# Kernel tuning notes

Hardware: AMD Instinct MI355X
Metric: run time of the kernel (lower is better)

The kernel has to match this reference:

```python
import jax, jax.numpy as jnp
import numpy as np

NUM_FORMULAS = 1024
INPUT_DIM = 256
BATCH = 2048


def setup_inputs() -> dict:
    key = jax.random.key(0)
    k_x, k_mu, k_sigma = jax.random.split(key, 3)
    inputs = jax.random.normal(k_x, (BATCH, INPUT_DIM), dtype=jnp.float32)
    # keras random_normal initializer default stddev = 0.05
    mu = 0.05 * jax.random.normal(k_mu, (NUM_FORMULAS, INPUT_DIM), dtype=jnp.float32)
    sigma = 0.05 * jax.random.normal(k_sigma, (1, NUM_FORMULAS, INPUT_DIM), dtype=jnp.float32)
    temperature = jnp.float32(2.0)
    return {"inputs": inputs, "mu": mu, "sigma": sigma, "temperature": temperature}


def reference(inputs, mu, sigma, temperature):
    # diff: (batch, num_formulas, dim)
    diff = inputs[:, None, :] - mu[None, :, :]
    # weighted L2 norm over feature dim -> (batch, num_formulas)
    dist = jnp.sqrt(jnp.sum(jnp.square(diff * sigma), axis=-1))
    loc = jnp.exp(-dist)
    # sigmoid-gated temperature, softmax over formulas (last axis)
    return jax.nn.softmax(jax.nn.sigmoid(temperature) * loc, axis=-1)
```

## Files before the change

kernel.cpp:

```cpp
#include <hip/hip_runtime.h>
#include <math.h>

#define NF 1024
#define DIM 256
#define BATCH 2048
#define K 512
#define BM 64
#define BN 64
#define KB 64
#define NCHUNK (NF / BN)

#define WS_A_BYTES (BATCH * K * 2)
#define WS_B_OFF   WS_A_BYTES
#define WS_C_OFF   (WS_A_BYTES + NF * K * 2)
#define WS_RP_OFF  (WS_C_OFF + NF * 4)

typedef __attribute__((ext_vector_type(8))) short short8;
typedef __attribute__((ext_vector_type(4))) float f32x4;

__device__ __forceinline__ unsigned short f2bf(float f) {
    unsigned u = __float_as_uint(f);
    u += 0x7fffu + ((u >> 16) & 1u);
    return (unsigned short)(u >> 16);
}

__device__ __forceinline__ void gl_lds16(const ushort* g, ushort* l) {
    __builtin_amdgcn_global_load_lds(
        (const __attribute__((address_space(1))) void*)g,
        (__attribute__((address_space(3))) void*)l, 16, 0, 0);
}

__global__ __launch_bounds__(256) void k_prep(const float* __restrict__ mu,
                                              const float* __restrict__ sigma,
                                              const float* __restrict__ x,
                                              unsigned int* __restrict__ Ab32,
                                              unsigned int* __restrict__ Bb32,
                                              float* __restrict__ c) {
    const int t = threadIdx.x;
    if (blockIdx.x >= NF) {
        const int i = (blockIdx.x - NF) * 256 + t;
        const float v = x[i];
        Ab32[i] = (unsigned)f2bf(v * v) | ((unsigned)f2bf(v) << 16);
        return;
    }
    const int f = blockIdx.x;
    const float m = mu[f * DIM + t];
    const float s = sigma[f * DIM + t];
    const float s2 = s * s;
    Bb32[f * DIM + t] = (unsigned)f2bf(s2) | ((unsigned)f2bf(-2.0f * s2 * m) << 16);

    float cp = s2 * m * m;
    #pragma unroll
    for (int off = 32; off > 0; off >>= 1) cp += __shfl_down(cp, off, 64);
    __shared__ float red[4];
    const int lane = t & 63, wv = t >> 6;
    if (lane == 0) red[wv] = cp;
    __syncthreads();
    if (t == 0) c[f] = red[0] + red[1] + red[2] + red[3];
}

__global__ __launch_bounds__(256, 2) void k_main(const ushort* __restrict__ Ab,
                                                 const ushort* __restrict__ Bb,
                                                 const float* __restrict__ c,
                                                 const float* __restrict__ temp,
                                                 float* __restrict__ out,
                                                 float* __restrict__ rowPartial) {
    const int t = threadIdx.x;
    const int w = t >> 6;
    const int lane = t & 63;
    const int m16 = lane & 15;
    const int q = lane >> 4;
    const int wr = w >> 1, wc = w & 1;
    const int r0 = blockIdx.x * BM;
    const int n0 = blockIdx.y * BN;

    __shared__ __align__(16) ushort lds[8192];
    __shared__ float sums[4][32];

    f32x4 acc[2][2];
    #pragma unroll
    for (int rt = 0; rt < 2; ++rt)
        #pragma unroll
        for (int ct = 0; ct < 2; ++ct) acc[rt][ct] = (f32x4){0.f, 0.f, 0.f, 0.f};

    int srow[2], skc[2];
    #pragma unroll
    for (int h = 0; h < 2; ++h) {
        const int s = h * 256 + t;
        srow[h] = s >> 3;
        skc[h] = (s & 7) ^ (srow[h] & 7);
    }

    for (int kb = 0; kb < K; kb += KB) {
        __syncthreads();
        #pragma unroll
        for (int h = 0; h < 2; ++h) {
            const int s = h * 256 + t;
            gl_lds16(Ab + (r0 + srow[h]) * K + kb + skc[h] * 8, &lds[s * 8]);
            gl_lds16(Bb + (n0 + srow[h]) * K + kb + skc[h] * 8, &lds[4096 + s * 8]);
        }
        __syncthreads();

        #pragma unroll
        for (int ks = 0; ks < KB; ks += 32) {
            const int kcq = (ks >> 3) + q;
            short8 av[2], bv[2];
            #pragma unroll
            for (int j = 0; j < 2; ++j) {
                const int ar = wr * 32 + j * 16 + m16;
                av[j] = *(const short8*)&lds[(ar * 8 + (kcq ^ (ar & 7))) * 8];
                const int fr = wc * 32 + j * 16 + m16;
                bv[j] = *(const short8*)&lds[4096 + (fr * 8 + (kcq ^ (fr & 7))) * 8];
            }
            #pragma unroll
            for (int rt = 0; rt < 2; ++rt)
                #pragma unroll
                for (int ct = 0; ct < 2; ++ct)
                    acc[rt][ct] = __builtin_amdgcn_mfma_f32_16x16x32_bf16(
                        av[rt], bv[ct], acc[rt][ct], 0, 0, 0);
        }
    }

    const float g = 1.0f / (1.0f + __expf(-temp[0]));
    #pragma unroll
    for (int rt = 0; rt < 2; ++rt) {
        float s[4] = {0.f, 0.f, 0.f, 0.f};
        #pragma unroll
        for (int ct = 0; ct < 2; ++ct) {
            const int fcol = n0 + wc * 32 + ct * 16 + m16;
            const float cn = c[fcol];
            #pragma unroll
            for (int i = 0; i < 4; ++i) {
                const float dist2 = acc[rt][ct][i] + cn;
                const float dist = sqrtf(fmaxf(dist2, 0.0f));
                const float p = __expf(g * __expf(-dist));
                const int row = r0 + wr * 32 + rt * 16 + q * 4 + i;
                out[row * NF + fcol] = p;
                s[i] += p;
            }
        }
        #pragma unroll
        for (int i = 0; i < 4; ++i) {
            #pragma unroll
            for (int mask = 1; mask < 16; mask <<= 1)
                s[i] += __shfl_xor(s[i], mask, 64);
        }
        if (m16 == 0) {
            #pragma unroll
            for (int i = 0; i < 4; ++i) sums[w][rt * 16 + q * 4 + i] = s[i];
        }
    }
    __syncthreads();
    if (t < BM) {
        const int half = t >> 5, lr = t & 31;
        rowPartial[blockIdx.y * BATCH + r0 + t] =
            sums[half * 2][lr] + sums[half * 2 + 1][lr];
    }
}

__global__ __launch_bounds__(256) void k_norm(float* __restrict__ out,
                                              const float* __restrict__ rowPartial) {
    const int row = blockIdx.x;
    float ssum = 0.0f;
    #pragma unroll
    for (int ch = 0; ch < NCHUNK; ++ch) ssum += rowPartial[ch * BATCH + row];
    const float inv = 1.0f / ssum;
    float4* o4 = (float4*)(out + row * NF);
    float4 v = o4[threadIdx.x];
    v.x *= inv; v.y *= inv; v.z *= inv; v.w *= inv;
    o4[threadIdx.x] = v;
}

extern "C" void kernel_launch(void* const* d_in, const int* in_sizes, int n_in,
                              void* d_out, int out_size, void* d_ws, size_t ws_size,
                              hipStream_t stream) {
    const float* x     = (const float*)d_in[0];
    const float* mu    = (const float*)d_in[1];
    const float* sigma = (const float*)d_in[2];
    const float* temp  = (const float*)d_in[3];
    float* out = (float*)d_out;

    char* ws = (char*)d_ws;
    ushort* Ab        = (ushort*)ws;
    ushort* Bb        = (ushort*)(ws + WS_B_OFF);
    float*  c         = (float*)(ws + WS_C_OFF);
    float*  rowPartial = (float*)(ws + WS_RP_OFF);

    k_prep<<<NF + BATCH * DIM / 256, 256, 0, stream>>>(mu, sigma, x,
                                                       (unsigned int*)Ab,
                                                       (unsigned int*)Bb, c);

    dim3 g2(BATCH / BM, NF / BN);
    k_main<<<g2, 256, 0, stream>>>(Ab, Bb, c, temp, out, rowPartial);

    k_norm<<<BATCH, 256, 0, stream>>>(out, rowPartial);
}
```

Baseline: 80.26 us.

## Fuse softmax normalization into GEMM kernel with full-row blocks and in-kernel A conversion

Each block now computes 16 full output rows across all 1024 formulas, using 8 waves of 128 columns each. This lets the softmax row sum and normalization happen inside the kernel, which removes the separate normalize kernel and the extra read and rewrite of the output. The x-to-bf16 packing moves from the prep kernel into the main kernel's LDS staging. B operands are read straight from global memory into registers with double buffering instead of going through LDS tiles. The risk is heavy redundant B traffic (every block reads the whole 1 MB B), served by L2. There are also fewer blocks (128) than CUs, which may underfill the GPU.

```diff
diff --git a/kernel.cpp b/kernel.cpp
--- a/kernel.cpp
+++ b/kernel.cpp
@@ -5,15 +5,10 @@
 #define DIM 256
 #define BATCH 2048
 #define K 512
-#define BM 64
-#define BN 64
-#define KB 64
-#define NCHUNK (NF / BN)
+#define BMF 16
+#define GX (BATCH / BMF)
 
-#define WS_A_BYTES (BATCH * K * 2)
-#define WS_B_OFF   WS_A_BYTES
-#define WS_C_OFF   (WS_A_BYTES + NF * K * 2)
-#define WS_RP_OFF  (WS_C_OFF + NF * 4)
+#define WS_C_OFF (NF * K * 2)
 
 typedef __attribute__((ext_vector_type(8))) short short8;
 typedef __attribute__((ext_vector_type(4))) float f32x4;
@@ -24,25 +19,11 @@
     return (unsigned short)(u >> 16);
 }
 
-__device__ __forceinline__ void gl_lds16(const ushort* g, ushort* l) {
-    __builtin_amdgcn_global_load_lds(
-        (const __attribute__((address_space(1))) void*)g,
-        (__attribute__((address_space(3))) void*)l, 16, 0, 0);
-}
-
 __global__ __launch_bounds__(256) void k_prep(const float* __restrict__ mu,
                                               const float* __restrict__ sigma,
-                                              const float* __restrict__ x,
-                                              unsigned int* __restrict__ Ab32,
                                               unsigned int* __restrict__ Bb32,
                                               float* __restrict__ c) {
     const int t = threadIdx.x;
-    if (blockIdx.x >= NF) {
-        const int i = (blockIdx.x - NF) * 256 + t;
-        const float v = x[i];
-        Ab32[i] = (unsigned)f2bf(v * v) | ((unsigned)f2bf(v) << 16);
-        return;
-    }
     const int f = blockIdx.x;
     const float m = mu[f * DIM + t];
     const float s = sigma[f * DIM + t];
@@ -59,116 +40,131 @@
     if (t == 0) c[f] = red[0] + red[1] + red[2] + red[3];
 }
 
-__global__ __launch_bounds__(256, 2) void k_main(const ushort* __restrict__ Ab,
+__global__ __launch_bounds__(512, 2) void k_full(const float* __restrict__ x,
                                                  const ushort* __restrict__ Bb,
                                                  const float* __restrict__ c,
                                                  const float* __restrict__ temp,
-                                                 float* __restrict__ out,
-                                                 float* __restrict__ rowPartial) {
+                                                 float* __restrict__ out) {
     const int t = threadIdx.x;
     const int w = t >> 6;
     const int lane = t & 63;
     const int m16 = lane & 15;
     const int q = lane >> 4;
-    const int wr = w >> 1, wc = w & 1;
-    const int r0 = blockIdx.x * BM;
-    const int n0 = blockIdx.y * BN;
+    const int r0 = blockIdx.x * BMF;
 
-    __shared__ __align__(16) ushort lds[8192];
-    __shared__ float sums[4][32];
+    __shared__ __align__(16) ushort ldsA[BMF * K];
+    __shared__ float wsum[8][BMF];
+    __shared__ float rowInv[BMF];
 
-    f32x4 acc[2][2];
-    #pragma unroll
-    for (int rt = 0; rt < 2; ++rt)
-        #pragma unroll
-        for (int ct = 0; ct < 2; ++ct) acc[rt][ct] = (f32x4){0.f, 0.f, 0.f, 0.f};
-
-    int srow[2], skc[2];
     #pragma unroll
     for (int h = 0; h < 2; ++h) {
-        const int s = h * 256 + t;
-        srow[h] = s >> 3;
-        skc[h] = (s & 7) ^ (srow[h] & 7);
+        const int u = h * 512 + t;
+        const int row = u >> 6, kc = u & 63;
+        const float4 v = *(const float4*)&x[(r0 + row) * DIM + kc * 4];
+        uint4 pk;
+        pk.x = (unsigned)f2bf(v.x * v.x) | ((unsigned)f2bf(v.x) << 16);
+        pk.y = (unsigned)f2bf(v.y * v.y) | ((unsigned)f2bf(v.y) << 16);
+        pk.z = (unsigned)f2bf(v.z * v.z) | ((unsigned)f2bf(v.z) << 16);
+        pk.w = (unsigned)f2bf(v.w * v.w) | ((unsigned)f2bf(v.w) << 16);
+        *(uint4*)&ldsA[(row * 64 + (kc ^ (row & 7))) * 8] = pk;
     }
+    __syncthreads();
 
-    for (int kb = 0; kb < K; kb += KB) {
-        __syncthreads();
+    f32x4 acc[8];
+    #pragma unroll
+    for (int ct = 0; ct < 8; ++ct) acc[ct] = (f32x4){0.f, 0.f, 0.f, 0.f};
+
+    const ushort* bbase = Bb + (w * 128 + m16) * K + q * 8;
+
+    short8 b0[8], b1[8];
+    #pragma unroll
+    for (int ct = 0; ct < 8; ++ct)
+        b0[ct] = *(const short8*)(bbase + ct * 16 * K);
+
+    #pragma unroll 1
+    for (int n = 0; n < 14; n += 2) {
         #pragma unroll
-        for (int h = 0; h < 2; ++h) {
-            const int s = h * 256 + t;
-            gl_lds16(Ab + (r0 + srow[h]) * K + kb + skc[h] * 8, &lds[s * 8]);
-            gl_lds16(Bb + (n0 + srow[h]) * K + kb + skc[h] * 8, &lds[4096 + s * 8]);
+        for (int ct = 0; ct < 8; ++ct)
+            b1[ct] = *(const short8*)(bbase + ct * 16 * K + (n + 1) * 32);
+        {
+            const int kcq = (n << 2) + q;
+            const short8 av = *(const short8*)&ldsA[(m16 * 64 + (kcq ^ (m16 & 7))) * 8];
+            #pragma unroll
+            for (int ct = 0; ct < 8; ++ct)
+                acc[ct] = __builtin_amdgcn_mfma_f32_16x16x32_bf16(av, b0[ct], acc[ct], 0, 0, 0);
         }
-        __syncthreads();
-
         #pragma unroll
-        for (int ks = 0; ks < KB; ks += 32) {
-            const int kcq = (ks >> 3) + q;
-            short8 av[2], bv[2];
+        for (int ct = 0; ct < 8; ++ct)
+            b0[ct] = *(const short8*)(bbase + ct * 16 * K + (n + 2) * 32);
+        {
+            const int kcq = ((n + 1) << 2) + q;
+            const short8 av = *(const short8*)&ldsA[(m16 * 64 + (kcq ^ (m16 & 7))) * 8];
             #pragma unroll
-            for (int j = 0; j < 2; ++j) {
-                const int ar = wr * 32 + j * 16 + m16;
-                av[j] = *(const short8*)&lds[(ar * 8 + (kcq ^ (ar & 7))) * 8];
-                const int fr = wc * 32 + j * 16 + m16;
-                bv[j] = *(const short8*)&lds[4096 + (fr * 8 + (kcq ^ (fr & 7))) * 8];
-            }
-            #pragma unroll
-            for (int rt = 0; rt < 2; ++rt)
-                #pragma unroll
-                for (int ct = 0; ct < 2; ++ct)
-                    acc[rt][ct] = __builtin_amdgcn_mfma_f32_16x16x32_bf16(
-                        av[rt], bv[ct], acc[rt][ct], 0, 0, 0);
+            for (int ct = 0; ct < 8; ++ct)
+                acc[ct] = __builtin_amdgcn_mfma_f32_16x16x32_bf16(av, b1[ct], acc[ct], 0, 0, 0);
         }
+    }
+    #pragma unroll
+    for (int ct = 0; ct < 8; ++ct)
+        b1[ct] = *(const short8*)(bbase + ct * 16 * K + 15 * 32);
+    {
+        const int kcq = 56 + q;
+        const short8 av = *(const short8*)&ldsA[(m16 * 64 + (kcq ^ (m16 & 7))) * 8];
+        #pragma unroll
+        for (int ct = 0; ct < 8; ++ct)
+            acc[ct] = __builtin_amdgcn_mfma_f32_16x16x32_bf16(av, b0[ct], acc[ct], 0, 0, 0);
+    }
+    {
+        const int kcq = 60 + q;
+        const short8 av = *(const short8*)&ldsA[(m16 * 64 + (kcq ^ (m16 & 7))) * 8];
+        #pragma unroll
+        for (int ct = 0; ct < 8; ++ct)
+            acc[ct] = __builtin_amdgcn_mfma_f32_16x16x32_bf16(av, b1[ct], acc[ct], 0, 0, 0);
     }
 
     const float g = 1.0f / (1.0f + __expf(-temp[0]));
+    float s[4] = {0.f, 0.f, 0.f, 0.f};
     #pragma unroll
-    for (int rt = 0; rt < 2; ++rt) {
-        float s[4] = {0.f, 0.f, 0.f, 0.f};
-        #pragma unroll
-        for (int ct = 0; ct < 2; ++ct) {
-            const int fcol = n0 + wc * 32 + ct * 16 + m16;
-            const float cn = c[fcol];
-            #pragma unroll
-            for (int i = 0; i < 4; ++i) {
-                const float dist2 = acc[rt][ct][i] + cn;
-                const float dist = sqrtf(fmaxf(dist2, 0.0f));
-                const float p = __expf(g * __expf(-dist));
-                const int row = r0 + wr * 32 + rt * 16 + q * 4 + i;
-                out[row * NF + fcol] = p;
-                s[i] += p;
-            }
-        }
+    for (int ct = 0; ct < 8; ++ct) {
+        const float cn = c[w * 128 + ct * 16 + m16];
         #pragma unroll
         for (int i = 0; i < 4; ++i) {
-            #pragma unroll
-            for (int mask = 1; mask < 16; mask <<= 1)
-                s[i] += __shfl_xor(s[i], mask, 64);
-        }
-        if (m16 == 0) {
-            #pragma unroll
-            for (int i = 0; i < 4; ++i) sums[w][rt * 16 + q * 4 + i] = s[i];
+            const float dist2 = acc[ct][i] + cn;
+            const float dist = sqrtf(fmaxf(dist2, 0.0f));
+            const float p = __expf(g * __expf(-dist));
+            acc[ct][i] = p;
+            s[i] += p;
         }
     }
+    #pragma unroll
+    for (int i = 0; i < 4; ++i) {
+        #pragma unroll
+        for (int mask = 1; mask < 16; mask <<= 1)
+            s[i] += __shfl_xor(s[i], mask, 64);
+    }
+    if (m16 == 0) {
+        #pragma unroll
+        for (int i = 0; i < 4; ++i) wsum[w][q * 4 + i] = s[i];
+    }
     __syncthreads();
-    if (t < BM) {
-        const int half = t >> 5, lr = t & 31;
-        rowPartial[blockIdx.y * BATCH + r0 + t] =
-            sums[half * 2][lr] + sums[half * 2 + 1][lr];
+    if (t < BMF) {
+        float ssum = 0.f;
+        #pragma unroll
+        for (int ww = 0; ww < 8; ++ww) ssum += wsum[ww][t];
+        rowInv[t] = 1.0f / ssum;
     }
-}
+    __syncthreads();
 
-__global__ __launch_bounds__(256) void k_norm(float* __restrict__ out,
-                                              const float* __restrict__ rowPartial) {
-    const int row = blockIdx.x;
-    float ssum = 0.0f;
+    float inv[4];
     #pragma unroll
-    for (int ch = 0; ch < NCHUNK; ++ch) ssum += rowPartial[ch * BATCH + row];
-    const float inv = 1.0f / ssum;
-    float4* o4 = (float4*)(out + row * NF);
-    float4 v = o4[threadIdx.x];
-    v.x *= inv; v.y *= inv; v.z *= inv; v.w *= inv;
-    o4[threadIdx.x] = v;
+    for (int i = 0; i < 4; ++i) inv[i] = rowInv[q * 4 + i];
+    #pragma unroll
+    for (int ct = 0; ct < 8; ++ct) {
+        const int fcol = w * 128 + ct * 16 + m16;
+        #pragma unroll
+        for (int i = 0; i < 4; ++i)
+            out[(r0 + q * 4 + i) * NF + fcol] = acc[ct][i] * inv[i];
+    }
 }
 
 extern "C" void kernel_launch(void* const* d_in, const int* in_sizes, int n_in,
@@ -181,17 +177,9 @@
     float* out = (float*)d_out;
 
     char* ws = (char*)d_ws;
-    ushort* Ab        = (ushort*)ws;
-    ushort* Bb        = (ushort*)(ws + WS_B_OFF);
-    float*  c         = (float*)(ws + WS_C_OFF);
-    float*  rowPartial = (float*)(ws + WS_RP_OFF);
+    ushort* Bb = (ushort*)ws;
+    float*  c  = (float*)(ws + WS_C_OFF);
 
-    k_prep<<<NF + BATCH * DIM / 256, 256, 0, stream>>>(mu, sigma, x,
-                                                       (unsigned int*)Ab,
-                                                       (unsigned int*)Bb, c);
-
-    dim3 g2(BATCH / BM, NF / BN);
-    k_main<<<g2, 256, 0, stream>>>(Ab, Bb, c, temp, out, rowPartial);
-
-    k_norm<<<BATCH, 256, 0, stream>>>(out, rowPartial);
+    k_prep<<<NF, 256, 0, stream>>>(mu, sigma, (unsigned int*)Bb, c);
+    k_full<<<GX, 512, 0, stream>>>(x, Bb, c, temp, out);
 }
```

Result: slower. 97.36 us (+21.3%).
